# Optimization experiments

Hardware: AMD Instinct MI355X
Metric: run time of the kernel (lower is better)

Reference implementation:

```python
import math
import jax, jax.numpy as jnp
import numpy as np

ALPHA = 1000.0
N_LAMBDA = 1.0


def setup_inputs() -> dict:
    key = jax.random.key(0)
    k1, k2 = jax.random.split(key)
    xyz1 = jax.random.normal(k1, (4, 8192, 3), dtype=jnp.float32)  # prediction
    xyz2 = jax.random.normal(k2, (4, 8192, 3), dtype=jnp.float32)  # ground truth
    return {"xyz1": xyz1, "xyz2": xyz2}


def _nn(a, b):
    """For each point in a [B,Na,3], squared dist + index of nearest point in b [B,Nb,3]."""
    a2 = jnp.sum(a * a, axis=-1)[:, :, None]          # [B,Na,1]
    b2 = jnp.sum(b * b, axis=-1)[:, None, :]          # [B,1,Nb]
    d = a2 + b2 - 2.0 * jnp.einsum('bnd,bmd->bnm', a, b)  # [B,Na,Nb]
    return jnp.min(d, axis=-1), jnp.argmin(d, axis=-1)


def reference(xyz1, xyz2):
    B, n_x, _ = xyz1.shape
    n_gt = xyz2.shape[1]
    frac_21 = n_gt / n_x

    # torch code calls ChamferFunction.apply(xyz2, xyz1):
    # dist1/idx1 are for gt points (idx1 indexes into xyz1, range n_x),
    # dist2/idx2 are for pred points (idx2 indexes into xyz2, range n_gt).
    dist1, idx1 = _nn(xyz2, xyz1)   # [B, n_gt]
    dist2, idx2 = _nn(xyz1, xyz2)   # [B, n_x]

    exp_dist1 = jnp.exp(-dist1 * ALPHA)
    exp_dist2 = jnp.exp(-dist2 * ALPHA)

    batch = jnp.arange(B)[:, None]

    # how many gt points picked each pred point
    count1 = jnp.zeros((B, n_x), jnp.int32).at[batch, idx1].add(1)
    weight1 = jnp.take_along_axis(count1, idx1, axis=1).astype(jnp.float32) ** N_LAMBDA
    weight1 = 1.0 / jnp.maximum(frac_21 / weight1 + 1e-6, 1.0)
    loss1 = jnp.mean(1.0 - exp_dist1 * weight1, axis=1)

    # how many pred points picked each gt point
    count2 = jnp.zeros((B, n_gt), jnp.int32).at[batch, idx2].add(1)
    weight2 = jnp.take_along_axis(count2, idx2, axis=1).astype(jnp.float32) ** N_LAMBDA
    weight2 = 1.0 / (math.ceil(frac_21) * weight2 + 1e-6)
    loss2 = jnp.mean(1.0 - exp_dist2 * weight2, axis=1)

    return jnp.mean((loss1 + loss2) / 2.0)
```

## Files before the change

kernel.cpp:

```cpp
#include <hip/hip_runtime.h>
#include <cstdint>
#include <cstddef>

#define BATCH 4
#define NPTS 8192
#define CHUNK 128
#define BLOCK 256
#define QPT 8
#define QPB (BLOCK * QPT)
#define NKEYS (2 * BATCH * NPTS)

typedef float v2f __attribute__((ext_vector_type(2)));

__device__ __forceinline__ float halfnorm(float px, float py, float pz) {
    return 0.5f * fmaf(pz, pz, fmaf(py, py, px * px));
}
__device__ __forceinline__ float score(float qx, float qy, float qz,
                                       float px, float py, float pz, float ph) {
    float t = fmaf(-qx, px, ph);
    t = fmaf(-qy, py, t);
    return fmaf(-qz, pz, t);
}
__device__ __forceinline__ unsigned int mono_f32(float f) {
    unsigned int u = __float_as_uint(f);
    return u ^ (unsigned int)(((int)u >> 31) | 0x80000000);
}

__global__ void __launch_bounds__(BLOCK) prep_kernel(
        const float* __restrict__ xyz1,
        const float* __restrict__ xyz2,
        float* __restrict__ planes,
        unsigned int* __restrict__ counts,
        float* __restrict__ esum,
        float* __restrict__ out) {
    const int gtid = blockIdx.x * BLOCK + threadIdx.x;
    const int arr = gtid >> 15;
    const int rem = gtid & 32767;
    const int b = rem >> 13;
    const int i = rem & (NPTS - 1);
    const float* src = ((arr == 0) ? xyz1 : xyz2) + (size_t)(b * NPTS + i) * 3;
    const float px = src[0], py = src[1], pz = src[2];
    const size_t gb = ((size_t)(arr * 4 + b)) * 4 * NPTS;
    planes[gb + 0 * NPTS + i] = px;
    planes[gb + 1 * NPTS + i] = py;
    planes[gb + 2 * NPTS + i] = pz;
    planes[gb + 3 * NPTS + i] = halfnorm(px, py, pz);
    counts[gtid] = 0u;
    esum[gtid]   = 0.0f;
    if (gtid == 0) out[0] = 1.0f;
}

__global__ void __launch_bounds__(BLOCK, 4) nn_kernel(
        const float* __restrict__ xyz1,
        const float* __restrict__ xyz2,
        const float* __restrict__ planes,
        unsigned long long* __restrict__ keys) {
    const int tid = threadIdx.x;
    const int qt  = blockIdx.x;
    const int ct  = blockIdx.y;
    const int zb  = blockIdx.z;
    const int b   = zb & 3;
    const int dir = zb >> 2;
    const float* q_ptr = (dir == 0) ? xyz2 : xyz1;
    const int g = (dir == 0) ? b : 4 + b;
    const int chunk0 = ct * CHUNK;

    const float* Xp = planes + ((size_t)g * 4 + 0) * NPTS + chunk0;
    const float* Yp = planes + ((size_t)g * 4 + 1) * NPTS + chunk0;
    const float* Zp = planes + ((size_t)g * 4 + 2) * NPTS + chunk0;
    const float* Hp = planes + ((size_t)g * 4 + 3) * NPTS + chunk0;

    const int qbase = qt * QPB + tid;
    float qx[QPT], qy[QPT], qz[QPT];
#pragma unroll
    for (int u = 0; u < QPT; ++u) {
        const float* qp = q_ptr + (size_t)(b * NPTS + qbase + u * BLOCK) * 3;
        qx[u] = qp[0]; qy[u] = qp[1]; qz[u] = qp[2];
    }

    float bd[QPT];
    int   bj[QPT];
#pragma unroll
    for (int u = 0; u < QPT; ++u) { bd[u] = 3.4e38f; bj[u] = 0; }

#pragma unroll 2
    for (int j = 0; j < CHUNK; j += 8) {
        const v2f x01 = *(const v2f*)(Xp + j);
        const v2f x23 = *(const v2f*)(Xp + j + 2);
        const v2f x45 = *(const v2f*)(Xp + j + 4);
        const v2f x67 = *(const v2f*)(Xp + j + 6);
        const v2f y01 = *(const v2f*)(Yp + j);
        const v2f y23 = *(const v2f*)(Yp + j + 2);
        const v2f y45 = *(const v2f*)(Yp + j + 4);
        const v2f y67 = *(const v2f*)(Yp + j + 6);
        const v2f z01 = *(const v2f*)(Zp + j);
        const v2f z23 = *(const v2f*)(Zp + j + 2);
        const v2f z45 = *(const v2f*)(Zp + j + 4);
        const v2f z67 = *(const v2f*)(Zp + j + 6);
        const v2f h01 = *(const v2f*)(Hp + j);
        const v2f h23 = *(const v2f*)(Hp + j + 2);
        const v2f h45 = *(const v2f*)(Hp + j + 4);
        const v2f h67 = *(const v2f*)(Hp + j + 6);

#pragma unroll
        for (int u = 0; u < QPT; ++u) {
            const v2f nqx = {-qx[u], -qx[u]};
            const v2f nqy = {-qy[u], -qy[u]};
            const v2f nqz = {-qz[u], -qz[u]};
            v2f s01 = __builtin_elementwise_fma(nqx, x01, h01);
            v2f s23 = __builtin_elementwise_fma(nqx, x23, h23);
            v2f s45 = __builtin_elementwise_fma(nqx, x45, h45);
            v2f s67 = __builtin_elementwise_fma(nqx, x67, h67);
            s01 = __builtin_elementwise_fma(nqy, y01, s01);
            s23 = __builtin_elementwise_fma(nqy, y23, s23);
            s45 = __builtin_elementwise_fma(nqy, y45, s45);
            s67 = __builtin_elementwise_fma(nqy, y67, s67);
            s01 = __builtin_elementwise_fma(nqz, z01, s01);
            s23 = __builtin_elementwise_fma(nqz, z23, s23);
            s45 = __builtin_elementwise_fma(nqz, z45, s45);
            s67 = __builtin_elementwise_fma(nqz, z67, s67);

            float m0 = fminf(fminf(s01.x, s01.y), s23.x);
            float m1 = fminf(fminf(s23.y, s45.x), s45.y);
            float m2 = fminf(fminf(s67.x, s67.y), m0);
            float m  = fminf(m1, m2);
            if (m < bd[u]) { bd[u] = m; bj[u] = j; }
        }
    }

    const size_t base = ((size_t)zb) * NPTS;
#pragma unroll
    for (int u = 0; u < QPT; ++u) {
        unsigned long long key =
            ((unsigned long long)mono_f32(bd[u]) << 32) |
            (unsigned int)(chunk0 + bj[u]);
        atomicMin(&keys[base + qbase + u * BLOCK], key);
    }
}

__global__ void __launch_bounds__(BLOCK) mid_kernel(
        const float* __restrict__ xyz1,
        const float* __restrict__ xyz2,
        const unsigned long long* __restrict__ keys,
        unsigned int* __restrict__ counts,
        float* __restrict__ esum) {
    const int gtid = blockIdx.x * BLOCK + threadIdx.x;
    const int group = gtid >> 13;
    const int q   = gtid & (NPTS - 1);
    const int b   = group & 3;
    const int dir = group >> 2;
    const float* q_ptr = (dir == 0) ? xyz2 : xyz1;
    const float* d_ptr = (dir == 0) ? xyz1 : xyz2;

    const unsigned long long key = keys[gtid];
    const unsigned int smin_m = (unsigned int)(key >> 32);
    const int gbase = ((int)(unsigned int)key) & (NPTS - 8);

    const float* qp = q_ptr + (size_t)(b * NPTS + q) * 3;
    const float qx = qp[0], qy = qp[1], qz = qp[2];

    const float4* g4 = (const float4*)(d_ptr + (size_t)(b * NPTS + gbase) * 3);
    float4 t0 = g4[0], t1 = g4[1], t2 = g4[2], t3 = g4[3], t4 = g4[4], t5 = g4[5];
    float px[8] = {t0.x, t0.w, t1.z, t2.y, t3.x, t3.w, t4.z, t5.y};
    float py[8] = {t0.y, t1.x, t1.w, t2.z, t3.y, t4.x, t4.w, t5.z};
    float pz[8] = {t0.z, t1.y, t2.x, t2.w, t3.z, t4.y, t5.x, t5.w};

    int r = 0;
    float sx = px[0], sy = py[0], sz = pz[0];
#pragma unroll
    for (int k = 7; k >= 0; --k) {
        float ph = halfnorm(px[k], py[k], pz[k]);
        float s  = score(qx, qy, qz, px[k], py[k], pz[k], ph);
        if (mono_f32(s) == smin_m) { r = k; sx = px[k]; sy = py[k]; sz = pz[k]; }
    }
    const int idx = gbase + r;

    const float dx = qx - sx, dy = qy - sy, dz = qz - sz;
    const float d = dx * dx + dy * dy + dz * dz;
    const float e = expf(-1000.0f * d);

    atomicAdd(&counts[(size_t)group * NPTS + idx], 1u);
    atomicAdd(&esum[(size_t)group * NPTS + idx], e);
}

__global__ void __launch_bounds__(BLOCK) final_kernel(
        const unsigned int* __restrict__ counts,
        const float* __restrict__ esum,
        float* __restrict__ out) {
    __shared__ float red[4];
    const int gtid = blockIdx.x * BLOCK + threadIdx.x;
    const int dir = gtid >> 15;

    const float c = (float)counts[gtid];
    const float e = esum[gtid];
    float w;
    if (dir == 0) w = 1.0f / fmaxf(1.0f / c + 1e-6f, 1.0f);
    else          w = 1.0f / (c + 1e-6f);
    float term = -w * e;

#pragma unroll
    for (int off = 32; off > 0; off >>= 1)
        term += __shfl_down(term, off);
    const int lane = threadIdx.x & 63;
    const int wid  = threadIdx.x >> 6;
    if (lane == 0) red[wid] = term;
    __syncthreads();
    if (threadIdx.x == 0) {
        float t = red[0] + red[1] + red[2] + red[3];
        atomicAdd(out, t * (1.0f / 65536.0f));
    }
}

extern "C" void kernel_launch(void* const* d_in, const int* in_sizes, int n_in,
                              void* d_out, int out_size, void* d_ws, size_t ws_size,
                              hipStream_t stream) {
    const float* xyz1 = (const float*)d_in[0];
    const float* xyz2 = (const float*)d_in[1];
    float* out = (float*)d_out;

    unsigned long long* keys = (unsigned long long*)d_ws;
    unsigned int* counts = (unsigned int*)((char*)d_ws + (size_t)NKEYS * 8);
    float* esum = (float*)((char*)d_ws + (size_t)NKEYS * 12);
    float* planes = (float*)((char*)d_ws + (size_t)NKEYS * 16);

    prep_kernel<<<NKEYS / BLOCK, BLOCK, 0, stream>>>(xyz1, xyz2, planes,
                                                     counts, esum, out);
    nn_kernel<<<dim3(NPTS / QPB, NPTS / CHUNK, 2 * BATCH), BLOCK, 0, stream>>>(
        xyz1, xyz2, planes, keys);
    mid_kernel<<<NKEYS / BLOCK, BLOCK, 0, stream>>>(xyz1, xyz2, keys, counts, esum);
    final_kernel<<<NKEYS / BLOCK, BLOCK, 0, stream>>>(counts, esum, out);
}
```

Baseline: 108.5 us.

## Drop per-group index tracking in NN loop; rescan winning chunk in mid kernel

The hot nearest-neighbour loop no longer records which 8-point group held the minimum. It folds every score straight into a running fminf chain and removes the compare/select bookkeeping per query per step. The key now carries only the chunk base. The mid kernel rescans all 128 points of the winning chunk from the SoA planes to recover the exact index, which moves more work (128 score evaluations per query) into a small follow-up kernel. The serial fmin chain also lengthens the dependency chain within each unrolled iteration.

Result: slower. 159.5 us (+47.0%).

```diff
diff --git a/kernel.cpp b/kernel.cpp
--- a/kernel.cpp
+++ b/kernel.cpp
@@ -79,9 +79,8 @@
     }
 
     float bd[QPT];
-    int   bj[QPT];
-#pragma unroll
-    for (int u = 0; u < QPT; ++u) { bd[u] = 3.4e38f; bj[u] = 0; }
+#pragma unroll
+    for (int u = 0; u < QPT; ++u) bd[u] = 3.4e38f;
 
 #pragma unroll 2
     for (int j = 0; j < CHUNK; j += 8) {
@@ -120,11 +119,12 @@
             s45 = __builtin_elementwise_fma(nqz, z45, s45);
             s67 = __builtin_elementwise_fma(nqz, z67, s67);
 
-            float m0 = fminf(fminf(s01.x, s01.y), s23.x);
-            float m1 = fminf(fminf(s23.y, s45.x), s45.y);
-            float m2 = fminf(fminf(s67.x, s67.y), m0);
-            float m  = fminf(m1, m2);
-            if (m < bd[u]) { bd[u] = m; bj[u] = j; }
+            float m = bd[u];
+            m = fminf(fminf(m, s01.x), s01.y);
+            m = fminf(fminf(m, s23.x), s23.y);
+            m = fminf(fminf(m, s45.x), s45.y);
+            m = fminf(fminf(m, s67.x), s67.y);
+            bd[u] = m;
         }
     }
 
@@ -132,8 +132,7 @@
 #pragma unroll
     for (int u = 0; u < QPT; ++u) {
         unsigned long long key =
-            ((unsigned long long)mono_f32(bd[u]) << 32) |
-            (unsigned int)(chunk0 + bj[u]);
+            ((unsigned long long)mono_f32(bd[u]) << 32) | (unsigned int)chunk0;
         atomicMin(&keys[base + qbase + u * BLOCK], key);
     }
 }
@@ -141,6 +140,7 @@
 __global__ void __launch_bounds__(BLOCK) mid_kernel(
         const float* __restrict__ xyz1,
         const float* __restrict__ xyz2,
+        const float* __restrict__ planes,
         const unsigned long long* __restrict__ keys,
         unsigned int* __restrict__ counts,
         float* __restrict__ esum) {
@@ -150,30 +150,29 @@
     const int b   = group & 3;
     const int dir = group >> 2;
     const float* q_ptr = (dir == 0) ? xyz2 : xyz1;
-    const float* d_ptr = (dir == 0) ? xyz1 : xyz2;
+    const int g = (dir == 0) ? b : 4 + b;
 
     const unsigned long long key = keys[gtid];
     const unsigned int smin_m = (unsigned int)(key >> 32);
-    const int gbase = ((int)(unsigned int)key) & (NPTS - 8);
+    const int chunk0 = ((int)(unsigned int)key) & (NPTS - CHUNK);
 
     const float* qp = q_ptr + (size_t)(b * NPTS + q) * 3;
     const float qx = qp[0], qy = qp[1], qz = qp[2];
 
-    const float4* g4 = (const float4*)(d_ptr + (size_t)(b * NPTS + gbase) * 3);
-    float4 t0 = g4[0], t1 = g4[1], t2 = g4[2], t3 = g4[3], t4 = g4[4], t5 = g4[5];
-    float px[8] = {t0.x, t0.w, t1.z, t2.y, t3.x, t3.w, t4.z, t5.y};
-    float py[8] = {t0.y, t1.x, t1.w, t2.z, t3.y, t4.x, t4.w, t5.z};
-    float pz[8] = {t0.z, t1.y, t2.x, t2.w, t3.z, t4.y, t5.x, t5.w};
+    const float* Xp = planes + ((size_t)g * 4 + 0) * NPTS + chunk0;
+    const float* Yp = planes + ((size_t)g * 4 + 1) * NPTS + chunk0;
+    const float* Zp = planes + ((size_t)g * 4 + 2) * NPTS + chunk0;
+    const float* Hp = planes + ((size_t)g * 4 + 3) * NPTS + chunk0;
 
     int r = 0;
-    float sx = px[0], sy = py[0], sz = pz[0];
-#pragma unroll
-    for (int k = 7; k >= 0; --k) {
-        float ph = halfnorm(px[k], py[k], pz[k]);
-        float s  = score(qx, qy, qz, px[k], py[k], pz[k], ph);
-        if (mono_f32(s) == smin_m) { r = k; sx = px[k]; sy = py[k]; sz = pz[k]; }
-    }
-    const int idx = gbase + r;
+    float sx = Xp[0], sy = Yp[0], sz = Zp[0];
+#pragma unroll 4
+    for (int k = CHUNK - 1; k >= 0; --k) {
+        const float px = Xp[k], py = Yp[k], pz = Zp[k];
+        const float s = score(qx, qy, qz, px, py, pz, Hp[k]);
+        if (mono_f32(s) == smin_m) { r = k; sx = px; sy = py; sz = pz; }
+    }
+    const int idx = chunk0 + r;
 
     const float dx = qx - sx, dy = qy - sy, dz = qz - sz;
     const float d = dx * dx + dy * dy + dz * dz;
@@ -227,6 +226,7 @@
                                                      counts, esum, out);
     nn_kernel<<<dim3(NPTS / QPB, NPTS / CHUNK, 2 * BATCH), BLOCK, 0, stream>>>(
         xyz1, xyz2, planes, keys);
-    mid_kernel<<<NKEYS / BLOCK, BLOCK, 0, stream>>>(xyz1, xyz2, keys, counts, esum);
+    mid_kernel<<<NKEYS / BLOCK, BLOCK, 0, stream>>>(xyz1, xyz2, planes, keys,
+                                                    counts, esum);
     final_kernel<<<NKEYS / BLOCK, BLOCK, 0, stream>>>(counts, esum, out);
 }
```
